# Kernel optimization log

Hardware: AMD Instinct MI355X
Metric: run time of the kernel (lower is better)

## Reference

```python
import jax, jax.numpy as jnp
import numpy as np

B, S, IN, OUT = 4, 512, 1024, 512
T, G, K, R = 16, 2, 4, 32  # tables, groups, cells, rank
OUTPUT_SCALE = 1.0 / np.sqrt(T * G).astype(np.float32)


def setup_inputs() -> dict:
    key = jax.random.key(0)
    k0, k1, k2, k3 = jax.random.split(key, 4)
    x = jax.random.normal(k0, (B, S, IN), dtype=jnp.float32)
    proj_w = jax.random.normal(k1, (R, IN), dtype=jnp.float32) / np.sqrt(IN)
    router_w = jax.random.normal(k2, (T, G, K, R), dtype=jnp.float32) / np.sqrt(R)
    router_b = jnp.zeros((T, G, K), dtype=jnp.float32)
    affine_w = jax.random.normal(k3, (T, G, K, R, OUT), dtype=jnp.float32) * 0.02
    affine_b = jnp.zeros((T, G, K, OUT), dtype=jnp.float32)
    return {"x": x, "proj_w": proj_w, "router_w": router_w, "router_b": router_b,
            "affine_w": affine_w, "affine_b": affine_b}


def reference(x, proj_w, router_w, router_b, affine_w, affine_b):
    # z: (B,S,R) low-rank projection
    z = jnp.einsum('bsi,ri->bsr', x, proj_w)
    # routing scores per (table, group, cell): (B,S,T,G,K)
    scores = jnp.einsum('bsr,tgkr->bstgk', z, router_w) + router_b
    # per-cell affine outputs: (B,S,T,G,K,O) -- dominant intermediate
    cell_values = jnp.einsum('bsr,tgkro->bstgko', z, affine_w) + affine_b
    # tropical (min-plus) winner selection: argmin over cells
    winner = jnp.argmin(scores, axis=-1)  # (B,S,T,G)
    idx = jnp.broadcast_to(winner[..., None, None],
                           winner.shape + (1, cell_values.shape[-1]))
    group_output = jnp.take_along_axis(cell_values, idx, axis=4)[..., 0, :]  # (B,S,T,G,O)
    # sum over groups then tables, apply output scaling
    output = group_output.sum(axis=(2, 3)) * OUTPUT_SCALE  # (B,S,O)
    return output
```

## Files before the change

kernel.cpp:

```cpp
#include <hip/hip_runtime.h>

#define NTOK 2048
#define IN_DIM 1024
#define OUT_DIM 512
#define RNK 32
#define TG_N 32
#define TGK_N 128
#define AWCOLS 4096
#define KD 4224
#define NKT 66
#define SCALE_F 0.17677669529663687f

typedef __attribute__((ext_vector_type(8))) short short8;
typedef __attribute__((ext_vector_type(4))) float float4v;

__device__ __forceinline__ unsigned short f2bf(float f) {
  union { float f; unsigned int u; } c; c.f = f;
  unsigned int u = c.u;
  u += 0x7fffu + ((u >> 16) & 1u);
  return (unsigned short)(u >> 16);
}

__global__ __launch_bounds__(256) void k_zwin(
    const float* __restrict__ x, const float* __restrict__ proj_w,
    const float* __restrict__ router_w, const float* __restrict__ router_b,
    unsigned short* __restrict__ zout, unsigned long long* __restrict__ wout) {
  const int tok = blockIdx.x;
  const int t = threadIdx.x;
  __shared__ __align__(16) float zbuf[RNK];
  __shared__ float sc[TGK_N];
  __shared__ int winbuf[TG_N];

  const int r = t >> 3, c = t & 7;
  const float4* x4 = (const float4*)(x + (size_t)tok * IN_DIM);
  const float4* w4 = (const float4*)(proj_w + (size_t)r * IN_DIM);
  float acc = 0.f;
#pragma unroll
  for (int jj = 0; jj < 32; ++jj) {
    float4 xv = x4[jj * 8 + c];
    float4 wv = w4[jj * 8 + c];
    acc += xv.x * wv.x + xv.y * wv.y + xv.z * wv.z + xv.w * wv.w;
  }
  acc += __shfl_xor(acc, 1);
  acc += __shfl_xor(acc, 2);
  acc += __shfl_xor(acc, 4);
  if (c == 0) zbuf[r] = acc;
  __syncthreads();

  if (t < TGK_N) {
    const float4* rw = (const float4*)(router_w + (size_t)t * RNK);
    const float4* zb = (const float4*)zbuf;
    float s = router_b[t];
#pragma unroll
    for (int j = 0; j < 8; ++j) {
      float4 a = rw[j]; float4 b = zb[j];
      s += a.x * b.x + a.y * b.y + a.z * b.z + a.w * b.w;
    }
    sc[t] = s;
  }
  __syncthreads();

  if (t < TG_N) {
    float best = sc[t * 4]; int w = 0;
#pragma unroll
    for (int k = 1; k < 4; ++k) {
      float v = sc[t * 4 + k];
      if (v < best) { best = v; w = k; }
    }
    winbuf[t] = w;
  }
  if (t < RNK) zout[(size_t)tok * RNK + t] = f2bf(zbuf[t]);
  __syncthreads();
  if (t == 0) {
    unsigned long long w = 0ull;
    for (int g = 0; g < TG_N; ++g)
      w |= ((unsigned long long)(winbuf[g] & 3)) << (2 * g);
    wout[tok] = w;
  }
}

__global__ __launch_bounds__(256) void k_w2t(
    const float* __restrict__ aw, const float* __restrict__ ab,
    unsigned short* __restrict__ w2t) {
  __shared__ float tile[32][33];
  const int c0 = blockIdx.x * 32, o0 = blockIdx.y * 32;
  const int oo = threadIdx.x & 31, cc = threadIdx.x >> 5;
#pragma unroll
  for (int p = 0; p < 4; ++p) {
    int cidx = c0 + cc + p * 8;
    float v = (cidx < AWCOLS)
                  ? aw[(size_t)cidx * OUT_DIM + o0 + oo]
                  : ab[(size_t)(cidx - AWCOLS) * OUT_DIM + o0 + oo];
    tile[cc + p * 8][oo] = v;
  }
  __syncthreads();
  const int cc2 = threadIdx.x & 31, oo2 = threadIdx.x >> 5;
#pragma unroll
  for (int p = 0; p < 4; ++p) {
    int o = o0 + oo2 + p * 8;
    w2t[(size_t)o * KD + c0 + cc2] = f2bf(tile[cc2][oo2 + p * 8]);
  }
}

__global__ __launch_bounds__(256) void k_gemm(
    const unsigned short* __restrict__ z, const unsigned long long* __restrict__ win,
    const unsigned short* __restrict__ Bt, float* __restrict__ out) {
  __shared__ __align__(16) unsigned short Bs[2][32 * 64];
  const int bm = blockIdx.x, bn = blockIdx.y;
  const int tid = threadIdx.x;
  const int wave = tid >> 6, lane = tid & 63;
  const int l15 = lane & 15, quad = lane >> 4;
  const int mw = (wave & 1) * 32;
  const int nw = (wave >> 1) * 16;

  const int m0 = bm * 64 + mw + l15;
  const int m1 = m0 + 16;
  short8 z0 = *(const short8*)(z + (size_t)m0 * RNK + quad * 8);
  short8 z1 = *(const short8*)(z + (size_t)m1 * RNK + quad * 8);
  const unsigned long long w0 = win[m0], w1 = win[m1];

  const int nloc = wave * 8 + (lane >> 3);
  const int schunk = (lane & 7) ^ ((lane >> 3) & 7);
  const unsigned short* bsrc = Bt + (size_t)(bn * 32 + nloc) * KD + schunk * 8;

  float4v acc0 = {}, acc1 = {};
  const int nb = nw + l15;
  const int nrow = nb * 64;

  __builtin_amdgcn_global_load_lds(
      (const __attribute__((address_space(1))) void*)bsrc,
      (__attribute__((address_space(3))) void*)(&Bs[0][wave * 512]), 16, 0, 0);

  for (int kt = 0; kt < NKT; ++kt) {
    if (kt + 1 < NKT) {
      __builtin_amdgcn_global_load_lds(
          (const __attribute__((address_space(1))) void*)(bsrc + (size_t)(kt + 1) * 64),
          (__attribute__((address_space(3))) void*)(&Bs[(kt + 1) & 1][wave * 512]),
          16, 0, 0);
      asm volatile("s_waitcnt vmcnt(1)" ::: "memory");
    } else {
      asm volatile("s_waitcnt vmcnt(0)" ::: "memory");
    }
    asm volatile("s_barrier" ::: "memory");

    const unsigned short* B0 = &Bs[kt & 1][0];
    if (kt < 64) {
      const int tg = kt >> 1;
      const unsigned int e0 = (unsigned int)(w0 >> (2 * tg)) & 3u;
      const unsigned int e1 = (unsigned int)(w1 >> (2 * tg)) & 3u;
#pragma unroll
      for (int s = 0; s < 2; ++s) {
        const unsigned int kk = (unsigned int)(((kt & 1) << 1) | s);
        short8 zz = {};
        short8 a0 = (e0 == kk) ? z0 : zz;
        short8 a1 = (e1 == kk) ? z1 : zz;
        short8 b = *(const short8*)(B0 + nrow + (((s * 4 + quad) ^ (nb & 7)) * 8));
        acc0 = __builtin_amdgcn_mfma_f32_16x16x32_bf16(a0, b, acc0, 0, 0, 0);
        acc1 = __builtin_amdgcn_mfma_f32_16x16x32_bf16(a1, b, acc1, 0, 0, 0);
      }
    } else {
#pragma unroll
      for (int s = 0; s < 2; ++s) {
        const int tgA = (kt - 64) * 16 + s * 8 + quad * 2;
        union { short8 v; unsigned long long q[2]; } fa, fb;
        fa.q[0] = 0x3F80ull << (((unsigned)(w0 >> (2 * tgA)) & 3u) * 16);
        fa.q[1] = 0x3F80ull << (((unsigned)(w0 >> (2 * (tgA + 1))) & 3u) * 16);
        fb.q[0] = 0x3F80ull << (((unsigned)(w1 >> (2 * tgA)) & 3u) * 16);
        fb.q[1] = 0x3F80ull << (((unsigned)(w1 >> (2 * (tgA + 1))) & 3u) * 16);
        short8 b = *(const short8*)(B0 + nrow + (((s * 4 + quad) ^ (nb & 7)) * 8));
        acc0 = __builtin_amdgcn_mfma_f32_16x16x32_bf16(fa.v, b, acc0, 0, 0, 0);
        acc1 = __builtin_amdgcn_mfma_f32_16x16x32_bf16(fb.v, b, acc1, 0, 0, 0);
      }
    }
    asm volatile("s_barrier" ::: "memory");
  }

  const int col = bn * 32 + nw + l15;
#pragma unroll
  for (int tm = 0; tm < 2; ++tm) {
    float4v a = tm ? acc1 : acc0;
    const int rowb = bm * 64 + mw + tm * 16 + quad * 4;
#pragma unroll
    for (int rg = 0; rg < 4; ++rg)
      out[(size_t)(rowb + rg) * OUT_DIM + col] = a[rg] * SCALE_F;
  }
}

extern "C" void kernel_launch(void* const* d_in, const int* in_sizes, int n_in,
                              void* d_out, int out_size, void* d_ws, size_t ws_size,
                              hipStream_t stream) {
  const float* x        = (const float*)d_in[0];
  const float* proj_w   = (const float*)d_in[1];
  const float* router_w = (const float*)d_in[2];
  const float* router_b = (const float*)d_in[3];
  const float* affine_w = (const float*)d_in[4];
  const float* affine_b = (const float*)d_in[5];
  float* out = (float*)d_out;

  unsigned short* zout = (unsigned short*)d_ws;
  unsigned long long* wout = (unsigned long long*)((char*)d_ws + 131072);
  unsigned short* w2t = (unsigned short*)((char*)d_ws + 147456);

  k_w2t<<<dim3(KD / 32, OUT_DIM / 32), 256, 0, stream>>>(affine_w, affine_b, w2t);
  k_zwin<<<NTOK, 256, 0, stream>>>(x, proj_w, router_w, router_b, zout, wout);
  k_gemm<<<dim3(NTOK / 64, OUT_DIM / 32), 256, 0, stream>>>(zout, wout, w2t, out);
}
```

Baseline: 110.9 us.

## Fuse weight transpose with projection kernel and load GEMM B operand directly to registers

Merges the affine-weight transpose and the z/winner computation into one launch. Block ranges split the work, and each projection block now handles four tokens so every proj_w load is reused across them. The GEMM drops its LDS double-buffer and barriers and instead prefetches B fragments straight from global memory into registers two k-steps ahead. This removes a kernel launch and the barrier/LDS overhead, at the cost of uncoalesced-ish per-lane global loads and extra register pressure.

```diff
diff --git a/kernel.cpp b/kernel.cpp
--- a/kernel.cpp
+++ b/kernel.cpp
@@ -10,6 +10,7 @@
 #define KD 4224
 #define NKT 66
 #define SCALE_F 0.17677669529663687f
+#define W2T_BLOCKS 2112
 
 typedef __attribute__((ext_vector_type(8))) short short8;
 typedef __attribute__((ext_vector_type(4))) float float4v;
@@ -21,91 +22,108 @@
   return (unsigned short)(u >> 16);
 }
 
-__global__ __launch_bounds__(256) void k_zwin(
+__global__ __launch_bounds__(256) void k_prep(
+    const float* __restrict__ aw, const float* __restrict__ ab,
     const float* __restrict__ x, const float* __restrict__ proj_w,
     const float* __restrict__ router_w, const float* __restrict__ router_b,
+    unsigned short* __restrict__ w2t,
     unsigned short* __restrict__ zout, unsigned long long* __restrict__ wout) {
-  const int tok = blockIdx.x;
   const int t = threadIdx.x;
-  __shared__ __align__(16) float zbuf[RNK];
-  __shared__ float sc[TGK_N];
-  __shared__ int winbuf[TG_N];
-
+
+  if (blockIdx.x < W2T_BLOCKS) {
+    __shared__ float tile[32][33];
+    const int c0 = (blockIdx.x % 132) * 32, o0 = (blockIdx.x / 132) * 32;
+    const int oo = t & 31, cc = t >> 5;
+#pragma unroll
+    for (int p = 0; p < 4; ++p) {
+      int cidx = c0 + cc + p * 8;
+      float v = (cidx < AWCOLS)
+                    ? aw[(size_t)cidx * OUT_DIM + o0 + oo]
+                    : ab[(size_t)(cidx - AWCOLS) * OUT_DIM + o0 + oo];
+      tile[cc + p * 8][oo] = v;
+    }
+    __syncthreads();
+    const int cc2 = t & 31, oo2 = t >> 5;
+#pragma unroll
+    for (int p = 0; p < 4; ++p) {
+      int o = o0 + oo2 + p * 8;
+      w2t[(size_t)o * KD + c0 + cc2] = f2bf(tile[cc2][oo2 + p * 8]);
+    }
+    return;
+  }
+
+  __shared__ __align__(16) float zbuf[4][RNK];
+  __shared__ float sc[4][TGK_N];
+  __shared__ int winbuf[4][TG_N];
+  const int tok4 = (blockIdx.x - W2T_BLOCKS) * 4;
   const int r = t >> 3, c = t & 7;
-  const float4* x4 = (const float4*)(x + (size_t)tok * IN_DIM);
   const float4* w4 = (const float4*)(proj_w + (size_t)r * IN_DIM);
-  float acc = 0.f;
+  const float4* x0 = (const float4*)(x + (size_t)tok4 * IN_DIM);
+  float acc[4] = {0.f, 0.f, 0.f, 0.f};
 #pragma unroll
   for (int jj = 0; jj < 32; ++jj) {
-    float4 xv = x4[jj * 8 + c];
     float4 wv = w4[jj * 8 + c];
-    acc += xv.x * wv.x + xv.y * wv.y + xv.z * wv.z + xv.w * wv.w;
-  }
-  acc += __shfl_xor(acc, 1);
-  acc += __shfl_xor(acc, 2);
-  acc += __shfl_xor(acc, 4);
-  if (c == 0) zbuf[r] = acc;
+#pragma unroll
+    for (int tk = 0; tk < 4; ++tk) {
+      float4 xv = x0[tk * 256 + jj * 8 + c];
+      acc[tk] += xv.x * wv.x + xv.y * wv.y + xv.z * wv.z + xv.w * wv.w;
+    }
+  }
+#pragma unroll
+  for (int tk = 0; tk < 4; ++tk) {
+    float a = acc[tk];
+    a += __shfl_xor(a, 1);
+    a += __shfl_xor(a, 2);
+    a += __shfl_xor(a, 4);
+    if (c == 0) zbuf[tk][r] = a;
+  }
   __syncthreads();
 
-  if (t < TGK_N) {
-    const float4* rw = (const float4*)(router_w + (size_t)t * RNK);
-    const float4* zb = (const float4*)zbuf;
-    float s = router_b[t];
-#pragma unroll
-    for (int j = 0; j < 8; ++j) {
-      float4 a = rw[j]; float4 b = zb[j];
-      s += a.x * b.x + a.y * b.y + a.z * b.z + a.w * b.w;
-    }
-    sc[t] = s;
+  {
+    const int cell = t & 127, th = t >> 7;
+    const float4* rw = (const float4*)(router_w + (size_t)cell * RNK);
+    float4 a[8];
+#pragma unroll
+    for (int j = 0; j < 8; ++j) a[j] = rw[j];
+    const float rb = router_b[cell];
+#pragma unroll
+    for (int p = 0; p < 2; ++p) {
+      const int tk = th + p * 2;
+      const float4* zb = (const float4*)(&zbuf[tk][0]);
+      float s = rb;
+#pragma unroll
+      for (int j = 0; j < 8; ++j) {
+        float4 b = zb[j];
+        s += a[j].x * b.x + a[j].y * b.y + a[j].z * b.z + a[j].w * b.w;
+      }
+      sc[tk][cell] = s;
+    }
   }
   __syncthreads();
 
-  if (t < TG_N) {
-    float best = sc[t * 4]; int w = 0;
+  if (t < 128) {
+    const int tk = t >> 5, tg = t & 31;
+    float best = sc[tk][tg * 4]; int w = 0;
 #pragma unroll
     for (int k = 1; k < 4; ++k) {
-      float v = sc[t * 4 + k];
+      float v = sc[tk][tg * 4 + k];
       if (v < best) { best = v; w = k; }
     }
-    winbuf[t] = w;
-  }
-  if (t < RNK) zout[(size_t)tok * RNK + t] = f2bf(zbuf[t]);
+    winbuf[tk][tg] = w;
+    zout[(size_t)(tok4 + tk) * RNK + tg] = f2bf(zbuf[tk][tg]);
+  }
   __syncthreads();
-  if (t == 0) {
+  if (t < 4) {
     unsigned long long w = 0ull;
     for (int g = 0; g < TG_N; ++g)
-      w |= ((unsigned long long)(winbuf[g] & 3)) << (2 * g);
-    wout[tok] = w;
-  }
-}
-
-__global__ __launch_bounds__(256) void k_w2t(
-    const float* __restrict__ aw, const float* __restrict__ ab,
-    unsigned short* __restrict__ w2t) {
-  __shared__ float tile[32][33];
-  const int c0 = blockIdx.x * 32, o0 = blockIdx.y * 32;
-  const int oo = threadIdx.x & 31, cc = threadIdx.x >> 5;
-#pragma unroll
-  for (int p = 0; p < 4; ++p) {
-    int cidx = c0 + cc + p * 8;
-    float v = (cidx < AWCOLS)
-                  ? aw[(size_t)cidx * OUT_DIM + o0 + oo]
-                  : ab[(size_t)(cidx - AWCOLS) * OUT_DIM + o0 + oo];
-    tile[cc + p * 8][oo] = v;
-  }
-  __syncthreads();
-  const int cc2 = threadIdx.x & 31, oo2 = threadIdx.x >> 5;
-#pragma unroll
-  for (int p = 0; p < 4; ++p) {
-    int o = o0 + oo2 + p * 8;
-    w2t[(size_t)o * KD + c0 + cc2] = f2bf(tile[cc2][oo2 + p * 8]);
+      w |= ((unsigned long long)(winbuf[t][g] & 3)) << (2 * g);
+    wout[tok4 + t] = w;
   }
 }
 
 __global__ __launch_bounds__(256) void k_gemm(
     const unsigned short* __restrict__ z, const unsigned long long* __restrict__ win,
     const unsigned short* __restrict__ Bt, float* __restrict__ out) {
-  __shared__ __align__(16) unsigned short Bs[2][32 * 64];
   const int bm = blockIdx.x, bn = blockIdx.y;
   const int tid = threadIdx.x;
   const int wave = tid >> 6, lane = tid & 63;
@@ -119,45 +137,30 @@
   short8 z1 = *(const short8*)(z + (size_t)m1 * RNK + quad * 8);
   const unsigned long long w0 = win[m0], w1 = win[m1];
 
-  const int nloc = wave * 8 + (lane >> 3);
-  const int schunk = (lane & 7) ^ ((lane >> 3) & 7);
-  const unsigned short* bsrc = Bt + (size_t)(bn * 32 + nloc) * KD + schunk * 8;
+  const unsigned short* bp = Bt + (size_t)(bn * 32 + nw + l15) * KD + quad * 8;
 
   float4v acc0 = {}, acc1 = {};
-  const int nb = nw + l15;
-  const int nrow = nb * 64;
-
-  __builtin_amdgcn_global_load_lds(
-      (const __attribute__((address_space(1))) void*)bsrc,
-      (__attribute__((address_space(3))) void*)(&Bs[0][wave * 512]), 16, 0, 0);
-
+  short8 c0a = *(const short8*)(bp + 0);
+  short8 c0b = *(const short8*)(bp + 32);
+  short8 c1a = *(const short8*)(bp + 64);
+  short8 c1b = *(const short8*)(bp + 96);
+
+#pragma unroll 2
   for (int kt = 0; kt < NKT; ++kt) {
-    if (kt + 1 < NKT) {
-      __builtin_amdgcn_global_load_lds(
-          (const __attribute__((address_space(1))) void*)(bsrc + (size_t)(kt + 1) * 64),
-          (__attribute__((address_space(3))) void*)(&Bs[(kt + 1) & 1][wave * 512]),
-          16, 0, 0);
-      asm volatile("s_waitcnt vmcnt(1)" ::: "memory");
-    } else {
-      asm volatile("s_waitcnt vmcnt(0)" ::: "memory");
-    }
-    asm volatile("s_barrier" ::: "memory");
-
-    const unsigned short* B0 = &Bs[kt & 1][0];
+    const int kf = (kt + 2 < NKT) ? kt + 2 : NKT - 1;
+    short8 pa = *(const short8*)(bp + (size_t)kf * 64);
+    short8 pb = *(const short8*)(bp + (size_t)kf * 64 + 32);
+
     if (kt < 64) {
       const int tg = kt >> 1;
-      const unsigned int e0 = (unsigned int)(w0 >> (2 * tg)) & 3u;
-      const unsigned int e1 = (unsigned int)(w1 >> (2 * tg)) & 3u;
-#pragma unroll
-      for (int s = 0; s < 2; ++s) {
-        const unsigned int kk = (unsigned int)(((kt & 1) << 1) | s);
-        short8 zz = {};
-        short8 a0 = (e0 == kk) ? z0 : zz;
-        short8 a1 = (e1 == kk) ? z1 : zz;
-        short8 b = *(const short8*)(B0 + nrow + (((s * 4 + quad) ^ (nb & 7)) * 8));
-        acc0 = __builtin_amdgcn_mfma_f32_16x16x32_bf16(a0, b, acc0, 0, 0, 0);
-        acc1 = __builtin_amdgcn_mfma_f32_16x16x32_bf16(a1, b, acc1, 0, 0, 0);
-      }
+      const unsigned e0 = (unsigned)(w0 >> (2 * tg)) & 3u;
+      const unsigned e1 = (unsigned)(w1 >> (2 * tg)) & 3u;
+      const unsigned kk0 = (unsigned)((kt & 1) << 1), kk1 = kk0 | 1u;
+      short8 zz = {};
+      acc0 = __builtin_amdgcn_mfma_f32_16x16x32_bf16(e0 == kk0 ? z0 : zz, c0a, acc0, 0, 0, 0);
+      acc1 = __builtin_amdgcn_mfma_f32_16x16x32_bf16(e1 == kk0 ? z1 : zz, c0a, acc1, 0, 0, 0);
+      acc0 = __builtin_amdgcn_mfma_f32_16x16x32_bf16(e0 == kk1 ? z0 : zz, c0b, acc0, 0, 0, 0);
+      acc1 = __builtin_amdgcn_mfma_f32_16x16x32_bf16(e1 == kk1 ? z1 : zz, c0b, acc1, 0, 0, 0);
     } else {
 #pragma unroll
       for (int s = 0; s < 2; ++s) {
@@ -167,12 +170,12 @@
         fa.q[1] = 0x3F80ull << (((unsigned)(w0 >> (2 * (tgA + 1))) & 3u) * 16);
         fb.q[0] = 0x3F80ull << (((unsigned)(w1 >> (2 * tgA)) & 3u) * 16);
         fb.q[1] = 0x3F80ull << (((unsigned)(w1 >> (2 * (tgA + 1))) & 3u) * 16);
-        short8 b = *(const short8*)(B0 + nrow + (((s * 4 + quad) ^ (nb & 7)) * 8));
+        short8 b = s ? c0b : c0a;
         acc0 = __builtin_amdgcn_mfma_f32_16x16x32_bf16(fa.v, b, acc0, 0, 0, 0);
         acc1 = __builtin_amdgcn_mfma_f32_16x16x32_bf16(fb.v, b, acc1, 0, 0, 0);
       }
     }
-    asm volatile("s_barrier" ::: "memory");
+    c0a = c1a; c0b = c1b; c1a = pa; c1b = pb;
   }
 
   const int col = bn * 32 + nw + l15;
@@ -201,7 +204,7 @@
   unsigned long long* wout = (unsigned long long*)((char*)d_ws + 131072);
   unsigned short* w2t = (unsigned short*)((char*)d_ws + 147456);
 
-  k_w2t<<<dim3(KD / 32, OUT_DIM / 32), 256, 0, stream>>>(affine_w, affine_b, w2t);
-  k_zwin<<<NTOK, 256, 0, stream>>>(x, proj_w, router_w, router_b, zout, wout);
+  k_prep<<<W2T_BLOCKS + NTOK / 4, 256, 0, stream>>>(
+      affine_w, affine_b, x, proj_w, router_w, router_b, w2t, zout, wout);
   k_gemm<<<dim3(NTOK / 64, OUT_DIM / 32), 256, 0, stream>>>(zout, wout, w2t, out);
 }
```

Measured after the change: 134.6 us. +21.4%, slower.
